# Kernel tuning notes

Hardware: AMD Instinct MI355X
Metric: run time of the kernel (lower is better)

Reference implementation:

```python
import jax, jax.numpy as jnp
import numpy as np

B, S, D = 4, 4096, 64

def setup_inputs() -> dict:
    key = jax.random.key(0)
    ks = jax.random.split(key, 6)
    mk = lambda k: jax.random.normal(k, (B, S, D), dtype=jnp.float32)
    return {
        "q_re": mk(ks[0]), "q_im": mk(ks[1]),
        "k_re": mk(ks[2]), "k_im": mk(ks[3]),
        "v_re": mk(ks[4]), "v_im": mk(ks[5]),
    }

def reference(q_re, q_im, k_re, k_im, v_re, v_im):
    # Complex QK^T (no conjugate, matching torch.bmm on complex tensors):
    # (qr + i qi)(kr + i ki)^T -> re = qr kr^T - qi ki^T ; im = qr ki^T + qi kr^T
    d_k = q_re.shape[-1]
    scale = 1.0 / jnp.sqrt(jnp.asarray(d_k, dtype=q_re.dtype))
    s_re = (jnp.einsum('bqd,bkd->bqk', q_re, k_re)
            - jnp.einsum('bqd,bkd->bqk', q_im, k_im)) * scale
    s_im = (jnp.einsum('bqd,bkd->bqk', q_re, k_im)
            + jnp.einsum('bqd,bkd->bqk', q_im, k_re)) * scale
    # softmax over |scores| along key axis; weights are real (imag part is 0)
    w = jax.nn.softmax(jnp.sqrt(s_re * s_re + s_im * s_im), axis=-1)  # [B,S,S]
    # CVDropout is identity in eval mode. Output = real_weights @ complex_values
    o_re = jnp.einsum('bqk,bkd->bqd', w, v_re)
    o_im = jnp.einsum('bqk,bkd->bqd', w, v_im)
    return jnp.stack([o_re, o_im], axis=0)  # [2, B, S, D] (real, imag)
```

## Files before the change

### kernel.cpp

```cpp
#include <hip/hip_runtime.h>
#include <stdint.h>

#define B_    4
#define S_    4096
#define D_    64
#define QBLK  64
#define NELEM (B_ * S_ * D_)
#define BS_   (B_ * S_)

typedef __attribute__((ext_vector_type(8))) short bf16x8;
typedef __attribute__((ext_vector_type(4))) short bf16x4;
typedef __attribute__((ext_vector_type(4))) float f32x4;
typedef __attribute__((ext_vector_type(4))) int   i32x4;
typedef __attribute__((ext_vector_type(4))) unsigned u32x4;
typedef __attribute__((ext_vector_type(4))) _Float16 f16x4;

#define MFMA(a, b, c) __builtin_amdgcn_mfma_f32_16x16x32_bf16(a, b, c, 0, 0, 0)
#define VMWAIT(n) asm volatile("s_waitcnt vmcnt(" #n ")" ::: "memory")
#define BARRIER() do { asm volatile("" ::: "memory"); __builtin_amdgcn_s_barrier(); asm volatile("" ::: "memory"); } while (0)
#define LGKM_FENCE() do { asm volatile("s_waitcnt lgkmcnt(0)" ::: "memory"); __builtin_amdgcn_sched_barrier(0); } while (0)

__device__ __forceinline__ short f2bf(float x) {
    unsigned u = __builtin_bit_cast(unsigned, x);
    u += 0x7FFFu + ((u >> 16) & 1u);
    return (short)(u >> 16);
}

__device__ __forceinline__ unsigned cvtpk(float lo, float hi) {
    unsigned r;
    asm("v_cvt_pk_bf16_f32 %0, %1, %2" : "=v"(r) : "v"(lo), "v"(hi));
    return r;
}

__device__ __forceinline__ void async16(const short* g, short* l) {
    __builtin_amdgcn_global_load_lds(
        (const __attribute__((address_space(1))) unsigned int*)g,
        (__attribute__((address_space(3))) unsigned int*)l, 16, 0, 0);
}

__global__ __launch_bounds__(256)
void prepass_kernel(const float* __restrict__ q_re, const float* __restrict__ q_im,
                    const float* __restrict__ k_re, const float* __restrict__ k_im,
                    const float* __restrict__ v_re, const float* __restrict__ v_im,
                    short* __restrict__ ws) {
    const int bidx = blockIdx.x;
    const int tid  = threadIdx.x;
    if (bidx < 4096) {
        const int idx = bidx * 256 + tid;
        const int tn  = idx >> 18;
        const int e4  = idx & ((1 << 18) - 1);
        const float* s = (tn == 0 ? q_re : tn == 1 ? q_im : tn == 2 ? k_re : k_im)
                         + (size_t)e4 * 4;
        const float sc = (tn < 2) ? 0.125f : 1.0f;
        f32x4 x = *(const f32x4*)s;
        bf16x4 v;
#pragma unroll
        for (int c = 0; c < 4; ++c) v[c] = f2bf(x[c] * sc);
        *(bf16x4*)(ws + (size_t)tn * NELEM + (size_t)e4 * 4) = v;
    } else {
        __shared__ short tile[64][72];
        const int tb   = bidx - 4096;
        const int sb   = tb & 63;
        const int b    = (tb >> 6) & 3;
        const int comp = tb >> 8;
        const float* src = comp ? v_im : v_re;
        short* dst = ws + (size_t)(4 + comp) * NELEM;
#pragma unroll
        for (int i = 0; i < 4; ++i) {
            const int slot = i * 256 + tid;
            const int s  = slot >> 4;
            const int d4 = slot & 15;
            f32x4 x = *(const f32x4*)(src + (((size_t)b * S_) + sb * 64 + s) * D_ + d4 * 4);
#pragma unroll
            for (int c = 0; c < 4; ++c) tile[d4 * 4 + c][s] = f2bf(x[c]);
        }
        __syncthreads();
#pragma unroll
        for (int i = 0; i < 2; ++i) {
            const int slot = i * 256 + tid;
            const int d = slot >> 3;
            const int m = slot & 7;
            const int a = m >> 2, hh = m & 3;
            bf16x8 v;
#pragma unroll
            for (int j = 0; j < 8; ++j)
                v[j] = tile[d][a * 32 + hh * 4 + ((j >> 2) << 4) + (j & 3)];
            *(bf16x8*)(dst + ((size_t)b * 64 + d) * S_ + sb * 64 + m * 8) = v;
        }
    }
}

template<int SPLIT, typename OT>
__global__ __launch_bounds__(256, 4)
void cv_attn_main(const short* __restrict__ wsb,
                  float* __restrict__ out,
                  OT* __restrict__ opart,
                  float* __restrict__ ml)
{
    __shared__ __align__(16) short smem[2 * 8192];

    const int tid  = threadIdx.x;
    const int lane = tid & 63;
    const int wv   = tid >> 6;
    const int l15  = lane & 15;
    const int h    = lane >> 4;

    int bid = blockIdx.x;
    const int nwg = B_ * 64 * SPLIT;
    bid = (bid & 7) * (nwg >> 3) + (bid >> 3);
    const int qb = bid & 63;
    const int sp = (bid >> 6) % SPLIT;
    const int b  = bid / (64 * SPLIT);

    const short* qr  = wsb;
    const short* qi  = wsb + (size_t)NELEM;
    const short* kr  = wsb + 2 * (size_t)NELEM;
    const short* ki  = wsb + 3 * (size_t)NELEM;
    const short* vrT = wsb + 4 * (size_t)NELEM;
    const short* viT = wsb + 5 * (size_t)NELEM;

    short* kb0 = smem + l15 * 64 + ((h ^ (l15 & 7)) << 3);
    short* kb1 = smem + l15 * 64 + (((h ^ 4) ^ (l15 & 7)) << 3);
    short* vb0 = smem + l15 * 32 + ((h ^ (l15 & 3)) << 3);

    const int qrow = qb * QBLK + wv * 16 + l15;
    const size_t qoff = ((size_t)b * S_ + qrow) * D_;
    bf16x8 fqr[2], fqi[2], fqn[2];
#pragma unroll
    for (int dh = 0; dh < 2; ++dh) {
        fqr[dh] = *(const bf16x8*)(qr + qoff + dh * 32 + h * 8);
        fqi[dh] = *(const bf16x8*)(qi + qoff + dh * 32 + h * 8);
        i32x4 n = __builtin_bit_cast(i32x4, fqi[dh]) ^ (int)0x80008000;
        fqn[dh] = __builtin_bit_cast(bf16x8, n);
    }

    f32x4 o_re[4], o_im[4];
#pragma unroll
    for (int i = 0; i < 4; ++i) {
        o_re[i] = (f32x4){0.f, 0.f, 0.f, 0.f};
        o_im[i] = (f32x4){0.f, 0.f, 0.f, 0.f};
    }
    float m_run = -1e30f, l_run = 0.f;
    const float L2E = 1.44269504088896f;

    const int kRow = wv * 8 + (lane >> 3);
    const int u8   = lane & 7;
    const int vD   = wv * 16 + (lane >> 2);
    const int u4   = lane & 3;
    constexpr int TPB = (S_ / 32) / SPLIT;

    auto stage = [&](int t, int DST) {
        const int kb = (sp * TPB + t) * 32;
        const size_t koff = ((size_t)b * S_ + kb + kRow) * 64 + ((u8 ^ (kRow & 7)) << 3);
        async16(kr + koff, smem + DST + wv * 512);
        async16(ki + koff, smem + DST + 2048 + wv * 512);
        const size_t voff = ((size_t)b * 64 + vD) * S_ + kb + ((u4 ^ (vD & 3)) << 3);
        async16(vrT + voff, smem + DST + 4096 + wv * 512);
        async16(viT + voff, smem + DST + 6144 + wv * 512);
    };

    auto body = [&](int t, int CUR, int OTH) {
        VMWAIT(0);
        LGKM_FENCE();
        BARRIER();
        if (t + 1 < TPB) stage(t + 1, OTH);

        f32x4 s_re[2], s_im[2];
#pragma unroll
        for (int c = 0; c < 2; ++c) {
            s_re[c] = (f32x4){0.f, 0.f, 0.f, 0.f};
            s_im[c] = (f32x4){0.f, 0.f, 0.f, 0.f};
        }
        __builtin_amdgcn_s_setprio(1);
#pragma unroll
        for (int c = 0; c < 2; ++c) {
            bf16x8 fkr0 = *(const bf16x8*)(kb0 + CUR + c * 1024);
            bf16x8 fkr1 = *(const bf16x8*)(kb1 + CUR + c * 1024);
            bf16x8 fki0 = *(const bf16x8*)(kb0 + CUR + 2048 + c * 1024);
            bf16x8 fki1 = *(const bf16x8*)(kb1 + CUR + 2048 + c * 1024);
            s_re[c] = MFMA(fkr0, fqr[0], s_re[c]);
            s_re[c] = MFMA(fkr1, fqr[1], s_re[c]);
            s_re[c] = MFMA(fki0, fqn[0], s_re[c]);
            s_re[c] = MFMA(fki1, fqn[1], s_re[c]);
            s_im[c] = MFMA(fki0, fqr[0], s_im[c]);
            s_im[c] = MFMA(fki1, fqr[1], s_im[c]);
            s_im[c] = MFMA(fkr0, fqi[0], s_im[c]);
            s_im[c] = MFMA(fkr1, fqi[1], s_im[c]);
        }
        __builtin_amdgcn_s_setprio(0);

#pragma unroll
        for (int c = 0; c < 2; ++c) {
            f32x4 g = s_re[c] * s_re[c] + s_im[c] * s_im[c];
#pragma unroll
            for (int r = 0; r < 4; ++r) s_re[c][r] = __builtin_amdgcn_sqrtf(g[r]);
        }
        float tmax = fmaxf(fmaxf(fmaxf(s_re[0][0], s_re[0][1]), fmaxf(s_re[0][2], s_re[0][3])),
                           fmaxf(fmaxf(s_re[1][0], s_re[1][1]), fmaxf(s_re[1][2], s_re[1][3])));
        tmax = fmaxf(tmax, __shfl_xor(tmax, 16));
        tmax = fmaxf(tmax, __shfl_xor(tmax, 32));

        if (__any(tmax > m_run + 8.0f)) {
            const float m_new = fmaxf(m_run, tmax);
            const float alpha = __builtin_amdgcn_exp2f((m_run - m_new) * L2E);
            l_run *= alpha;
#pragma unroll
            for (int i = 0; i < 4; ++i) { o_re[i] *= alpha; o_im[i] *= alpha; }
            m_run = m_new;
        }
        const float nm = -m_run * L2E;

#pragma unroll
        for (int c = 0; c < 2; ++c)
#pragma unroll
            for (int r = 0; r < 4; ++r)
                s_im[c][r] = __builtin_amdgcn_exp2f(__builtin_fmaf(s_re[c][r], L2E, nm));
        f32x4 ps = s_im[0] + s_im[1];
        l_run += (ps[0] + ps[1]) + (ps[2] + ps[3]);

        u32x4 w;
        w[0] = cvtpk(s_im[0][0], s_im[0][1]);
        w[1] = cvtpk(s_im[0][2], s_im[0][3]);
        w[2] = cvtpk(s_im[1][0], s_im[1][1]);
        w[3] = cvtpk(s_im[1][2], s_im[1][3]);
        bf16x8 pb = __builtin_bit_cast(bf16x8, w);

        __builtin_amdgcn_s_setprio(1);
#pragma unroll
        for (int dc = 0; dc < 4; ++dc) {
            bf16x8 av = *(const bf16x8*)(vb0 + CUR + 4096 + dc * 512);
            bf16x8 ai = *(const bf16x8*)(vb0 + CUR + 6144 + dc * 512);
            o_re[dc] = MFMA(av, pb, o_re[dc]);
            o_im[dc] = MFMA(ai, pb, o_im[dc]);
        }
        __builtin_amdgcn_s_setprio(0);
    };

    stage(0, 0);
    for (int tt = 0; tt < TPB; tt += 2) {
        body(tt,     0,    8192);
        body(tt + 1, 8192, 0);
    }

    float lt = l_run;
    lt += __shfl_xor(lt, 16);
    lt += __shfl_xor(lt, 32);
    const float inv = 1.0f / lt;

    float* ol = (float*)smem;

    OT* dst_re;
    OT* dst_im;
    if constexpr (SPLIT == 1) {
        dst_re = (OT*)out + ((size_t)b * S_ + qb * QBLK) * D_;
        dst_im = dst_re + (size_t)NELEM;
    } else {
        const size_t qo = ((size_t)b * S_ + qb * QBLK) * D_;
        dst_re = opart + ((size_t)sp * 2 + 0) * NELEM + qo;
        dst_im = opart + ((size_t)sp * 2 + 1) * NELEM + qo;
    }

    auto store_comp = [&](const f32x4 (&oc)[4], OT* og) {
        __syncthreads();
#pragma unroll
        for (int dc = 0; dc < 4; ++dc)
#pragma unroll
            for (int r = 0; r < 4; ++r)
                ol[(wv * 16 + l15) * 65 + dc * 16 + h * 4 + r] = oc[dc][r] * inv;
        __syncthreads();
#pragma unroll
        for (int i = 0; i < 4; ++i) {
            const int slot = i * 256 + tid;
            const int row  = slot >> 4;
            const int c4   = slot & 15;
            f32x4 v;
#pragma unroll
            for (int j = 0; j < 4; ++j) v[j] = ol[row * 65 + c4 * 4 + j];
            if constexpr (sizeof(OT) == 4) {
                *(f32x4*)((float*)og + (size_t)row * D_ + c4 * 4) = v;
            } else {
                f16x4 hv;
#pragma unroll
                for (int j = 0; j < 4; ++j) hv[j] = (_Float16)v[j];
                *(f16x4*)((_Float16*)og + (size_t)row * D_ + c4 * 4) = hv;
            }
        }
    };
    store_comp(o_re, dst_re);
    store_comp(o_im, dst_im);

    if constexpr (SPLIT > 1) {
        if (lane < 16) {
            const int row = qb * QBLK + wv * 16 + lane;
            const size_t mo = ((size_t)sp * BS_ + (size_t)b * S_ + row) * 2;
            ml[mo]     = m_run;
            ml[mo + 1] = lt;
        }
    }
}

template<int SPLIT, typename OT>
__global__ __launch_bounds__(256)
void cv_attn_combine(const OT* __restrict__ opart, const float* __restrict__ ml,
                     float* __restrict__ out) {
    const int idx  = blockIdx.x * 256 + threadIdx.x;
    const int d4   = idx & 15;
    const int rest = idx >> 4;
    const int row  = rest & (BS_ - 1);
    const int comp = rest >> 14;
    float ms[SPLIT], ls[SPLIT];
    float M = -1e30f;
#pragma unroll
    for (int s = 0; s < SPLIT; ++s) {
        ms[s] = ml[((size_t)s * BS_ + row) * 2];
        ls[s] = ml[((size_t)s * BS_ + row) * 2 + 1];
        M = fmaxf(M, ms[s]);
    }
    float W = 0.f;
    f32x4 acc = (f32x4){0.f, 0.f, 0.f, 0.f};
#pragma unroll
    for (int s = 0; s < SPLIT; ++s) {
        const float w = ls[s] * __builtin_amdgcn_exp2f((ms[s] - M) * 1.44269504088896f);
        W += w;
        const OT* op = opart + ((size_t)(s * 2 + comp)) * NELEM + (size_t)row * D_ + d4 * 4;
        f32x4 o;
        if constexpr (sizeof(OT) == 4) {
            o = *(const f32x4*)op;
        } else {
            f16x4 hv = *(const f16x4*)op;
#pragma unroll
            for (int j = 0; j < 4; ++j) o[j] = (float)hv[j];
        }
        acc += o * w;
    }
    acc *= (1.0f / W);
    *(f32x4*)(out + (size_t)comp * NELEM + (size_t)row * D_ + d4 * 4) = acc;
}

__global__ __launch_bounds__(256, 1)
void cv_attn_legacy(const float* __restrict__ q_re, const float* __restrict__ q_im,
                    const float* __restrict__ k_re, const float* __restrict__ k_im,
                    const float* __restrict__ v_re, const float* __restrict__ v_im,
                    float* __restrict__ out)
{
    __shared__ __align__(16) short smem[4 * 64 * D_];
    short* kr_s = smem;
    short* ki_s = smem + 4096;
    short* vr_s = smem + 8192;
    short* vi_s = smem + 12288;

    const int tid  = threadIdx.x;
    const int lane = tid & 63;
    const int wv   = tid >> 6;
    const int l15  = lane & 15;
    const int h    = lane >> 4;

    const int b  = blockIdx.x >> 6;
    const int qb = blockIdx.x & 63;
    const size_t boff = (size_t)b * S_ * D_;

    const int qrow = qb * QBLK + wv * 16 + l15;
    const float* qrp = q_re + boff + (size_t)qrow * D_;
    const float* qip = q_im + boff + (size_t)qrow * D_;
    bf16x8 fqr[2], fqi[2], fqn[2];
#pragma unroll
    for (int dh = 0; dh < 2; ++dh) {
        const int d0 = dh * 32 + h * 8;
        f32x4 a0 = *(const f32x4*)(qrp + d0);
        f32x4 a1 = *(const f32x4*)(qrp + d0 + 4);
        f32x4 b0 = *(const f32x4*)(qip + d0);
        f32x4 b1 = *(const f32x4*)(qip + d0 + 4);
#pragma unroll
        for (int j = 0; j < 4; ++j) {
            fqr[dh][j] = f2bf(a0[j]); fqr[dh][j + 4] = f2bf(a1[j]);
            fqi[dh][j] = f2bf(b0[j]); fqi[dh][j + 4] = f2bf(b1[j]);
            fqn[dh][j] = f2bf(-b0[j]); fqn[dh][j + 4] = f2bf(-b1[j]);
        }
    }

    f32x4 o_re[4], o_im[4];
#pragma unroll
    for (int i = 0; i < 4; ++i) {
        o_re[i] = (f32x4){0.f, 0.f, 0.f, 0.f};
        o_im[i] = (f32x4){0.f, 0.f, 0.f, 0.f};
    }
    float m_run = -1e30f, l_run = 0.f;
    const float SC = 0.125f * 1.44269504088896f;

    for (int t = 0; t < S_ / 64; ++t) {
        const int kb = t * 64;
#pragma unroll
        for (int a = 0; a < 2; ++a) {
            const float* src = (a ? k_im : k_re) + boff;
            short* dst = a ? ki_s : kr_s;
#pragma unroll
            for (int i = 0; i < 2; ++i) {
                const int slot = i * 256 + tid;
                const int row  = slot >> 3;
                const int cb   = slot & 7;
                const float* p = src + (size_t)(kb + row) * D_ + cb * 8;
                f32x4 x0 = *(const f32x4*)p;
                f32x4 x1 = *(const f32x4*)(p + 4);
                bf16x8 v;
#pragma unroll
                for (int j = 0; j < 4; ++j) { v[j] = f2bf(x0[j]); v[j + 4] = f2bf(x1[j]); }
                *(bf16x8*)(dst + row * 64 + ((cb ^ (row & 7)) << 3)) = v;
            }
        }
#pragma unroll
        for (int a = 0; a < 2; ++a) {
            const float* src = (a ? v_im : v_re) + boff;
            short* dst = a ? vi_s : vr_s;
#pragma unroll
            for (int i = 0; i < 4; ++i) {
                const int slot = i * 256 + tid;
                const int k  = slot >> 4;
                const int d4 = slot & 15;
                f32x4 x = *(const f32x4*)(src + (size_t)(kb + k) * D_ + d4 * 4);
#pragma unroll
                for (int c = 0; c < 4; ++c) {
                    const int d = d4 * 4 + c;
                    dst[d * 64 + (((k >> 2) ^ (d & 15)) << 2) + (k & 3)] = f2bf(x[c]);
                }
            }
        }
        __syncthreads();

        f32x4 s_re[4], s_im[4];
#pragma unroll
        for (int c = 0; c < 4; ++c) {
            s_re[c] = (f32x4){0.f, 0.f, 0.f, 0.f};
            s_im[c] = (f32x4){0.f, 0.f, 0.f, 0.f};
        }
#pragma unroll
        for (int c = 0; c < 4; ++c) {
            const int krow = c * 16 + l15;
#pragma unroll
            for (int dh = 0; dh < 2; ++dh) {
                const int u = ((dh * 4 + h) ^ (krow & 7)) << 3;
                bf16x8 fkr = *(const bf16x8*)(kr_s + krow * 64 + u);
                bf16x8 fki = *(const bf16x8*)(ki_s + krow * 64 + u);
                s_re[c] = MFMA(fkr, fqr[dh], s_re[c]);
                s_re[c] = MFMA(fki, fqn[dh], s_re[c]);
                s_im[c] = MFMA(fki, fqr[dh], s_im[c]);
                s_im[c] = MFMA(fkr, fqi[dh], s_im[c]);
            }
        }

        float pv[4][4];
        float tmax = 0.f;
#pragma unroll
        for (int c = 0; c < 4; ++c)
#pragma unroll
            for (int r = 0; r < 4; ++r) {
                const float re = s_re[c][r], im = s_im[c][r];
                const float mg = __builtin_amdgcn_sqrtf(re * re + im * im) * SC;
                pv[c][r] = mg;
                tmax = fmaxf(tmax, mg);
            }
        tmax = fmaxf(tmax, __shfl_xor(tmax, 16));
        tmax = fmaxf(tmax, __shfl_xor(tmax, 32));
        const float m_new = fmaxf(m_run, tmax);
        const float alpha = __builtin_amdgcn_exp2f(m_run - m_new);
        m_run = m_new;
        float psum = 0.f;
#pragma unroll
        for (int c = 0; c < 4; ++c)
#pragma unroll
            for (int r = 0; r < 4; ++r) {
                const float e = __builtin_amdgcn_exp2f(pv[c][r] - m_new);
                pv[c][r] = e;
                psum += e;
            }
        l_run = l_run * alpha + psum;
#pragma unroll
        for (int i = 0; i < 4; ++i) { o_re[i] *= alpha; o_im[i] *= alpha; }

        bf16x8 pb[2];
#pragma unroll
        for (int hf = 0; hf < 2; ++hf)
#pragma unroll
            for (int j = 0; j < 4; ++j) {
                pb[hf][j]     = f2bf(pv[hf * 2][j]);
                pb[hf][j + 4] = f2bf(pv[hf * 2 + 1][j]);
            }

#pragma unroll
        for (int hf = 0; hf < 2; ++hf) {
#pragma unroll
            for (int dc = 0; dc < 4; ++dc) {
                const int d  = dc * 16 + l15;
                const int s0 = (((hf * 8) + h)     ^ l15) << 2;
                const int s1 = (((hf * 8) + 4 + h) ^ l15) << 2;
                bf16x4 r0 = *(const bf16x4*)(vr_s + d * 64 + s0);
                bf16x4 r1 = *(const bf16x4*)(vr_s + d * 64 + s1);
                bf16x4 i0 = *(const bf16x4*)(vi_s + d * 64 + s0);
                bf16x4 i1 = *(const bf16x4*)(vi_s + d * 64 + s1);
                bf16x8 av, ai;
#pragma unroll
                for (int j = 0; j < 4; ++j) {
                    av[j] = r0[j]; av[j + 4] = r1[j];
                    ai[j] = i0[j]; ai[j + 4] = i1[j];
                }
                o_re[dc] = MFMA(av, pb[hf], o_re[dc]);
                o_im[dc] = MFMA(ai, pb[hf], o_im[dc]);
            }
        }
        __syncthreads();
    }

    float lt = l_run;
    lt += __shfl_xor(lt, 16);
    lt += __shfl_xor(lt, 32);
    const float inv = 1.0f / lt;

    float* ol = (float*)smem;
    auto store_comp = [&](const f32x4 (&oc)[4], float* og) {
#pragma unroll
        for (int dc = 0; dc < 4; ++dc)
#pragma unroll
            for (int r = 0; r < 4; ++r)
                ol[(wv * 16 + l15) * 65 + dc * 16 + h * 4 + r] = oc[dc][r] * inv;
        __syncthreads();
#pragma unroll
        for (int i = 0; i < 4; ++i) {
            const int slot = i * 256 + tid;
            const int row  = slot >> 4;
            const int c4   = slot & 15;
            f32x4 v;
#pragma unroll
            for (int j = 0; j < 4; ++j) v[j] = ol[row * 65 + c4 * 4 + j];
            *(f32x4*)(og + (size_t)row * D_ + c4 * 4) = v;
        }
        __syncthreads();
    };

    float* og0 = out + boff + (size_t)(qb * QBLK) * D_;
    store_comp(o_re, og0);
    store_comp(o_im, og0 + (size_t)B_ * S_ * D_);
}

extern "C" void kernel_launch(void* const* d_in, const int* in_sizes, int n_in,
                              void* d_out, int out_size, void* d_ws, size_t ws_size,
                              hipStream_t stream) {
    (void)in_sizes; (void)n_in; (void)out_size;
    const float* q_re = (const float*)d_in[0];
    const float* q_im = (const float*)d_in[1];
    const float* k_re = (const float*)d_in[2];
    const float* k_im = (const float*)d_in[3];
    const float* v_re = (const float*)d_in[4];
    const float* v_im = (const float*)d_in[5];
    float* out = (float*)d_out;

    const size_t bf_bytes = 6 * (size_t)NELEM * 2;
    const size_t mlsz     = 4 * (size_t)BS_ * 8;
    const size_t need4f16 = bf_bytes + 4 * 2 * (size_t)NELEM * 2 + mlsz;
    const size_t need4f32 = bf_bytes + 4 * 2 * (size_t)NELEM * 4 + mlsz;

    if (ws_size >= bf_bytes) {
        short* wsb = (short*)d_ws;
        prepass_kernel<<<4608, 256, 0, stream>>>(q_re, q_im, k_re, k_im, v_re, v_im, wsb);
        char* extra = (char*)d_ws + bf_bytes;
        if (ws_size >= need4f16) {
            _Float16* opart = (_Float16*)extra;
            float* ml = (float*)(extra + 4 * 2 * (size_t)NELEM * 2);
            cv_attn_main<4, _Float16><<<B_ * 64 * 4, 256, 0, stream>>>(wsb, nullptr, opart, ml);
            cv_attn_combine<4, _Float16><<<2048, 256, 0, stream>>>(opart, ml, out);
        } else if (ws_size >= need4f32) {
            float* opart = (float*)extra;
            float* ml    = (float*)(extra + 4 * 2 * (size_t)NELEM * 4);
            cv_attn_main<4, float><<<B_ * 64 * 4, 256, 0, stream>>>(wsb, nullptr, opart, ml);
            cv_attn_combine<4, float><<<2048, 256, 0, stream>>>(opart, ml, out);
        } else {
            cv_attn_main<1, float><<<B_ * 64, 256, 0, stream>>>(wsb, out, out, nullptr);
        }
    } else {
        cv_attn_legacy<<<B_ * 64, 256, 0, stream>>>(q_re, q_im, k_re, k_im, v_re, v_im, out);
    }
}
```

Baseline: 80.41 us.

## Software-pipeline QK of next tile under softmax·V, split keys eight ways

Result: slower. 91.45 us (+13.7%).

```diff
diff --git a/kernel.cpp b/kernel.cpp
--- a/kernel.cpp
+++ b/kernel.cpp
@@ -112,26 +112,22 @@
     const int sp = (bid >> 6) % SPLIT;
     const int b  = bid / (64 * SPLIT);
 
-    const short* qr  = wsb;
-    const short* qi  = wsb + (size_t)NELEM;
-    const short* kr  = wsb + 2 * (size_t)NELEM;
-    const short* ki  = wsb + 3 * (size_t)NELEM;
-    const short* vrT = wsb + 4 * (size_t)NELEM;
-    const short* viT = wsb + 5 * (size_t)NELEM;
-
-    short* kb0 = smem + l15 * 64 + ((h ^ (l15 & 7)) << 3);
-    short* kb1 = smem + l15 * 64 + (((h ^ 4) ^ (l15 & 7)) << 3);
-    short* vb0 = smem + l15 * 32 + ((h ^ (l15 & 3)) << 3);
+    const short* qr = wsb;
+    const short* qi = wsb + (size_t)NELEM;
+    const short* kr = wsb + 2 * (size_t)NELEM;
+    const short* ki = wsb + 3 * (size_t)NELEM;
+    const short* vT = wsb + 4 * (size_t)NELEM;
+
+    const short* p0 = smem + l15 * 64 + ((h ^ (l15 & 7)) << 3);
+    const short* p1 = smem + l15 * 64 + (((h ^ 4) ^ (l15 & 7)) << 3);
 
     const int qrow = qb * QBLK + wv * 16 + l15;
     const size_t qoff = ((size_t)b * S_ + qrow) * D_;
-    bf16x8 fqr[2], fqi[2], fqn[2];
+    bf16x8 fqr[2], fqi[2];
 #pragma unroll
     for (int dh = 0; dh < 2; ++dh) {
         fqr[dh] = *(const bf16x8*)(qr + qoff + dh * 32 + h * 8);
         fqi[dh] = *(const bf16x8*)(qi + qoff + dh * 32 + h * 8);
-        i32x4 n = __builtin_bit_cast(i32x4, fqi[dh]) ^ (int)0x80008000;
-        fqn[dh] = __builtin_bit_cast(bf16x8, n);
     }
 
     f32x4 o_re[4], o_im[4];
@@ -143,63 +139,67 @@
     float m_run = -1e30f, l_run = 0.f;
     const float L2E = 1.44269504088896f;
 
+    const int srcg = (lane & 7) ^ (lane >> 3);
     const int kRow = wv * 8 + (lane >> 3);
-    const int u8   = lane & 7;
-    const int vD   = wv * 16 + (lane >> 2);
-    const int u4   = lane & 3;
     constexpr int TPB = (S_ / 32) / SPLIT;
 
-    auto stage = [&](int t, int DST) {
+    auto stageK = [&](int t, int DST) {
         const int kb = (sp * TPB + t) * 32;
-        const size_t koff = ((size_t)b * S_ + kb + kRow) * 64 + ((u8 ^ (kRow & 7)) << 3);
+        const size_t koff = ((size_t)b * S_ + kb + kRow) * 64 + (srcg << 3);
         async16(kr + koff, smem + DST + wv * 512);
         async16(ki + koff, smem + DST + 2048 + wv * 512);
-        const size_t voff = ((size_t)b * 64 + vD) * S_ + kb + ((u4 ^ (vD & 3)) << 3);
-        async16(vrT + voff, smem + DST + 4096 + wv * 512);
-        async16(viT + voff, smem + DST + 6144 + wv * 512);
-    };
-
-    auto body = [&](int t, int CUR, int OTH) {
-        VMWAIT(0);
-        LGKM_FENCE();
-        BARRIER();
-        if (t + 1 < TPB) stage(t + 1, OTH);
-
-        f32x4 s_re[2], s_im[2];
+    };
+    auto stageV = [&](int t, int DST) {
+        const int kb = (sp * TPB + t) * 32;
+#pragma unroll
+        for (int i = 0; i < 2; ++i) {
+            const int d = (wv + 4 * i) * 8 + (lane >> 3);
+            const short* src = vT + ((srcg >> 2) ? (size_t)NELEM : (size_t)0)
+                               + ((size_t)b * 64 + d) * S_ + kb + (srcg & 3) * 8;
+            async16(src, smem + DST + 4096 + wv * 512 + i * 2048);
+        }
+    };
+
+    auto qk = [&](int CUR, f32x4 (&sre)[2], f32x4 (&sim)[2]) {
 #pragma unroll
         for (int c = 0; c < 2; ++c) {
-            s_re[c] = (f32x4){0.f, 0.f, 0.f, 0.f};
-            s_im[c] = (f32x4){0.f, 0.f, 0.f, 0.f};
-        }
+            sre[c] = (f32x4){0.f, 0.f, 0.f, 0.f};
+            sim[c] = (f32x4){0.f, 0.f, 0.f, 0.f};
+        }
+        i32x4 n0 = __builtin_bit_cast(i32x4, fqi[0]) ^ (int)0x80008000;
+        i32x4 n1 = __builtin_bit_cast(i32x4, fqi[1]) ^ (int)0x80008000;
+        bf16x8 fn0 = __builtin_bit_cast(bf16x8, n0);
+        bf16x8 fn1 = __builtin_bit_cast(bf16x8, n1);
         __builtin_amdgcn_s_setprio(1);
 #pragma unroll
         for (int c = 0; c < 2; ++c) {
-            bf16x8 fkr0 = *(const bf16x8*)(kb0 + CUR + c * 1024);
-            bf16x8 fkr1 = *(const bf16x8*)(kb1 + CUR + c * 1024);
-            bf16x8 fki0 = *(const bf16x8*)(kb0 + CUR + 2048 + c * 1024);
-            bf16x8 fki1 = *(const bf16x8*)(kb1 + CUR + 2048 + c * 1024);
-            s_re[c] = MFMA(fkr0, fqr[0], s_re[c]);
-            s_re[c] = MFMA(fkr1, fqr[1], s_re[c]);
-            s_re[c] = MFMA(fki0, fqn[0], s_re[c]);
-            s_re[c] = MFMA(fki1, fqn[1], s_re[c]);
-            s_im[c] = MFMA(fki0, fqr[0], s_im[c]);
-            s_im[c] = MFMA(fki1, fqr[1], s_im[c]);
-            s_im[c] = MFMA(fkr0, fqi[0], s_im[c]);
-            s_im[c] = MFMA(fkr1, fqi[1], s_im[c]);
+            bf16x8 a0 = *(const bf16x8*)(p0 + CUR + c * 1024);
+            bf16x8 a1 = *(const bf16x8*)(p1 + CUR + c * 1024);
+            bf16x8 b0 = *(const bf16x8*)(p0 + CUR + 2048 + c * 1024);
+            bf16x8 b1 = *(const bf16x8*)(p1 + CUR + 2048 + c * 1024);
+            sre[c] = MFMA(a0, fqr[0], sre[c]);
+            sre[c] = MFMA(a1, fqr[1], sre[c]);
+            sre[c] = MFMA(b0, fn0,    sre[c]);
+            sre[c] = MFMA(b1, fn1,    sre[c]);
+            sim[c] = MFMA(b0, fqr[0], sim[c]);
+            sim[c] = MFMA(b1, fqr[1], sim[c]);
+            sim[c] = MFMA(a0, fqi[0], sim[c]);
+            sim[c] = MFMA(a1, fqi[1], sim[c]);
         }
         __builtin_amdgcn_s_setprio(0);
-
+    };
+
+    auto spv = [&](int CUR, f32x4 (&sre)[2], f32x4 (&sim)[2]) {
 #pragma unroll
         for (int c = 0; c < 2; ++c) {
-            f32x4 g = s_re[c] * s_re[c] + s_im[c] * s_im[c];
-#pragma unroll
-            for (int r = 0; r < 4; ++r) s_re[c][r] = __builtin_amdgcn_sqrtf(g[r]);
-        }
-        float tmax = fmaxf(fmaxf(fmaxf(s_re[0][0], s_re[0][1]), fmaxf(s_re[0][2], s_re[0][3])),
-                           fmaxf(fmaxf(s_re[1][0], s_re[1][1]), fmaxf(s_re[1][2], s_re[1][3])));
+            f32x4 g = sre[c] * sre[c] + sim[c] * sim[c];
+#pragma unroll
+            for (int r = 0; r < 4; ++r) sre[c][r] = __builtin_amdgcn_sqrtf(g[r]);
+        }
+        float tmax = fmaxf(fmaxf(fmaxf(sre[0][0], sre[0][1]), fmaxf(sre[0][2], sre[0][3])),
+                           fmaxf(fmaxf(sre[1][0], sre[1][1]), fmaxf(sre[1][2], sre[1][3])));
         tmax = fmaxf(tmax, __shfl_xor(tmax, 16));
         tmax = fmaxf(tmax, __shfl_xor(tmax, 32));
-
         if (__any(tmax > m_run + 8.0f)) {
             const float m_new = fmaxf(m_run, tmax);
             const float alpha = __builtin_amdgcn_exp2f((m_run - m_new) * L2E);
@@ -209,37 +209,57 @@
             m_run = m_new;
         }
         const float nm = -m_run * L2E;
-
 #pragma unroll
         for (int c = 0; c < 2; ++c)
 #pragma unroll
             for (int r = 0; r < 4; ++r)
-                s_im[c][r] = __builtin_amdgcn_exp2f(__builtin_fmaf(s_re[c][r], L2E, nm));
-        f32x4 ps = s_im[0] + s_im[1];
+                sim[c][r] = __builtin_amdgcn_exp2f(__builtin_fmaf(sre[c][r], L2E, nm));
+        f32x4 ps = sim[0] + sim[1];
         l_run += (ps[0] + ps[1]) + (ps[2] + ps[3]);
 
         u32x4 w;
-        w[0] = cvtpk(s_im[0][0], s_im[0][1]);
-        w[1] = cvtpk(s_im[0][2], s_im[0][3]);
-        w[2] = cvtpk(s_im[1][0], s_im[1][1]);
-        w[3] = cvtpk(s_im[1][2], s_im[1][3]);
+        w[0] = cvtpk(sim[0][0], sim[0][1]);
+        w[1] = cvtpk(sim[0][2], sim[0][3]);
+        w[2] = cvtpk(sim[1][0], sim[1][1]);
+        w[3] = cvtpk(sim[1][2], sim[1][3]);
         bf16x8 pb = __builtin_bit_cast(bf16x8, w);
 
         __builtin_amdgcn_s_setprio(1);
 #pragma unroll
         for (int dc = 0; dc < 4; ++dc) {
-            bf16x8 av = *(const bf16x8*)(vb0 + CUR + 4096 + dc * 512);
-            bf16x8 ai = *(const bf16x8*)(vb0 + CUR + 6144 + dc * 512);
+            bf16x8 av = *(const bf16x8*)(p0 + CUR + 4096 + dc * 1024);
+            bf16x8 ai = *(const bf16x8*)(p1 + CUR + 4096 + dc * 1024);
             o_re[dc] = MFMA(av, pb, o_re[dc]);
             o_im[dc] = MFMA(ai, pb, o_im[dc]);
         }
         __builtin_amdgcn_s_setprio(0);
     };
 
-    stage(0, 0);
-    for (int tt = 0; tt < TPB; tt += 2) {
-        body(tt,     0,    8192);
-        body(tt + 1, 8192, 0);
+    auto body = [&](int t, int CUR, int NXT,
+                    f32x4 (&cre)[2], f32x4 (&cim)[2],
+                    f32x4 (&nre)[2], f32x4 (&nim)[2]) {
+        VMWAIT(0);
+        LGKM_FENCE();
+        BARRIER();
+        if (t + 2 < TPB) stageK(t + 2, CUR);
+        if (t + 1 < TPB) {
+            stageV(t + 1, NXT);
+            qk(NXT, nre, nim);
+        }
+        spv(CUR, cre, cim);
+    };
+
+    f32x4 sAre[2], sAim[2], sBre[2], sBim[2];
+    stageK(0, 0);
+    stageV(0, 0);
+    stageK(1, 8192);
+    VMWAIT(0);
+    BARRIER();
+    qk(0, sAre, sAim);
+
+    for (int t = 0; t < TPB; t += 2) {
+        body(t,     0,    8192, sAre, sAim, sBre, sBim);
+        body(t + 1, 8192, 0,    sBre, sBim, sAre, sAim);
     }
 
     float lt = l_run;
@@ -553,24 +573,23 @@
     float* out = (float*)d_out;
 
     const size_t bf_bytes = 6 * (size_t)NELEM * 2;
-    const size_t mlsz     = 4 * (size_t)BS_ * 8;
-    const size_t need4f16 = bf_bytes + 4 * 2 * (size_t)NELEM * 2 + mlsz;
-    const size_t need4f32 = bf_bytes + 4 * 2 * (size_t)NELEM * 4 + mlsz;
+    const size_t need8f16 = bf_bytes + 8 * 2 * (size_t)NELEM * 2 + 8 * (size_t)BS_ * 8;
+    const size_t need4f16 = bf_bytes + 4 * 2 * (size_t)NELEM * 2 + 4 * (size_t)BS_ * 8;
 
     if (ws_size >= bf_bytes) {
         short* wsb = (short*)d_ws;
         prepass_kernel<<<4608, 256, 0, stream>>>(q_re, q_im, k_re, k_im, v_re, v_im, wsb);
         char* extra = (char*)d_ws + bf_bytes;
-        if (ws_size >= need4f16) {
+        if (ws_size >= need8f16) {
+            _Float16* opart = (_Float16*)extra;
+            float* ml = (float*)(extra + 8 * 2 * (size_t)NELEM * 2);
+            cv_attn_main<8, _Float16><<<B_ * 64 * 8, 256, 0, stream>>>(wsb, nullptr, opart, ml);
+            cv_attn_combine<8, _Float16><<<2048, 256, 0, stream>>>(opart, ml, out);
+        } else if (ws_size >= need4f16) {
             _Float16* opart = (_Float16*)extra;
             float* ml = (float*)(extra + 4 * 2 * (size_t)NELEM * 2);
             cv_attn_main<4, _Float16><<<B_ * 64 * 4, 256, 0, stream>>>(wsb, nullptr, opart, ml);
             cv_attn_combine<4, _Float16><<<2048, 256, 0, stream>>>(opart, ml, out);
-        } else if (ws_size >= need4f32) {
-            float* opart = (float*)extra;
-            float* ml    = (float*)(extra + 4 * 2 * (size_t)NELEM * 4);
-            cv_attn_main<4, float><<<B_ * 64 * 4, 256, 0, stream>>>(wsb, nullptr, opart, ml);
-            cv_attn_combine<4, float><<<2048, 256, 0, stream>>>(opart, ml, out);
         } else {
             cv_attn_main<1, float><<<B_ * 64, 256, 0, stream>>>(wsb, out, out, nullptr);
         }
```
